# Kernel tuning notes

Hardware: AMD Instinct MI355X
Metric: run time of the kernel (lower is better)

## Reference

```python
import jax, jax.numpy as jnp
import numpy as np

NEG_BIG = -9.0e15


def masked_mean_softmax(idx):
    # softmax over a 0/-inf mask == uniform weights over positions where idx > 0
    logits = jnp.where(idx > 0, 1.0, NEG_BIG).astype(jnp.float32)
    return jax.nn.softmax(logits, axis=1)


def setup_inputs() -> dict:
    key = jax.random.key(0)
    ks = jax.random.split(key, 8)
    N_NODES, N_EDGES, EDGE_ARITY, NODE_DEG = 100000, 50000, 32, 16
    D_IN, D_OUT, TV = 128, 128, 128
    stdv = 1.0 / np.sqrt(D_IN)
    u = lambda k, shp: jax.random.uniform(k, shp, jnp.float32, -stdv, stdv)
    return {
        "x": jax.random.normal(ks[0], (N_NODES, D_IN), jnp.float32),
        "seq": jax.random.randint(ks[1], (N_EDGES, EDGE_ARITY), 0, N_NODES),
        "useq": jax.random.randint(ks[2], (N_NODES, NODE_DEG), 0, N_EDGES),
        "TextVector": jax.random.normal(ks[3], (TV,), jnp.float32),
        "weight1": u(ks[4], (D_IN, D_OUT)),
        "weight2": u(ks[5], (D_OUT, D_OUT)),
        "weight3": u(ks[6], (TV, TV)),
    }


def reference(x, seq, useq, TextVector, weight1, weight2, weight3):
    # NOTE: the torch module overwrites TextVector with weight3[0]; dropout is
    # a no-op in eval mode and is omitted here.
    tv = weight3[0]                                   # [TV]
    dot = weight3 @ tv                                # [TV]
    cos = dot / (jnp.linalg.norm(tv) * jnp.linalg.norm(weight3, axis=1))
    inter_nw = jnp.mean(cos)                          # scalar

    xw = (x @ weight1) * inter_nw                     # [N, D_OUT]

    nor = masked_mean_softmax(seq)                    # [E, A]
    adj_with_fea = xw[seq]                            # [E, A, D_OUT] gather
    edge = jnp.einsum('eac,ea->ec', adj_with_fea, nor)
    edge = jax.nn.relu(edge)
    e1 = edge @ weight2                               # [E, D_OUT]

    u_nor = masked_mean_softmax(useq)                 # [N, K]
    edge_adj = e1[useq]                               # [N, K, D_OUT] gather
    node = jnp.einsum('nkc,nk->nc', edge_adj, u_nor)  # [N, D_OUT]
    return node
```

## Files before the change

### kernel.cpp

```cpp
#include <hip/hip_runtime.h>
#include <hip/hip_fp16.h>

#define ND 100000
#define NE 50000
#define AR 32
#define DG 16
#define D  128

typedef _Float16 half8_t __attribute__((ext_vector_type(8)));
typedef _Float16 half4_t __attribute__((ext_vector_type(4)));
typedef float    f32x4_t __attribute__((ext_vector_type(4)));
typedef int      i32x4_t __attribute__((ext_vector_type(4)));

#define APAD 136

template<int OFF, int NI>
__device__ __forceinline__ void g_load8(half8_t (&v)[8], const int (&idxs)[NI],
                                        const _Float16* __restrict__ tab) {
    #pragma unroll
    for (int i = 0; i < 8; ++i)
        v[i] = *(const half8_t*)(tab + (size_t)idxs[OFF + i] * 32);
}

template<int OFF, int NI>
__device__ __forceinline__ void g_acc8(const half8_t (&v)[8], const int (&idxs)[NI],
                                       bool allv, float wv, float (&acc)[8]) {
    #pragma unroll
    for (int i = 0; i < 8; ++i) {
        float w = (allv | (idxs[OFF + i] > 0)) ? wv : 0.f;
        #pragma unroll
        for (int jj = 0; jj < 8; ++jj)
            acc[jj] = fmaf(w, (float)v[i][jj], acc[jj]);
    }
}

__global__ __launch_bounds__(256) void k_prep(const float* __restrict__ w1,
                                              const float* __restrict__ w2,
                                              const float* __restrict__ w3,
                                              _Float16* __restrict__ w1f,
                                              _Float16* __restrict__ w2f,
                                              float* __restrict__ inter_out) {
    if (blockIdx.x == 64) {
        __shared__ float red[128];
        int j = threadIdx.x;
        if (j < 128) {
            float dot = 0.f, sq = 0.f, sq0 = 0.f;
            #pragma unroll 8
            for (int k = 0; k < D; ++k) {
                float wj = w3[j * D + k];
                float w0 = w3[k];
                dot += wj * w0;
                sq  += wj * wj;
                sq0 += w0 * w0;
            }
            red[j] = dot / (sqrtf(sq0) * sqrtf(sq));
        }
        __syncthreads();
        if (j == 0) {
            float s = 0.f;
            for (int i = 0; i < 128; ++i) s += red[i];
            inter_out[0] = s / 128.f;
        }
        return;
    }
    int o = blockIdx.x * 256 + threadIdx.x;
    int j    = o & 7;
    int lane = (o >> 3) & 63;
    int frag = o >> 9;
    int ntile = frag >> 2, ktile = frag & 3;
    int n = ntile * 16 + (lane & 15);
    int k = ktile * 32 + (lane >> 4) * 8 + j;
    w1f[o] = (_Float16)w1[k * D + n];
    w2f[o] = (_Float16)w2[k * D + n];
}

__global__ __launch_bounds__(256) void k_xw(const float* __restrict__ x,
                                            const _Float16* __restrict__ w1f_g,
                                            const float* __restrict__ inter_p,
                                            _Float16* __restrict__ xws) {
    __shared__ _Float16 wfrag[D * D];
    __shared__ _Float16 xs[64 * APAD];
    int t = threadIdx.x;
    {
        const float4* src = (const float4*)w1f_g;
        float4* dst = (float4*)wfrag;
        #pragma unroll
        for (int i = 0; i < 8; ++i) dst[i * 256 + t] = src[i * 256 + t];
    }
    int rowbase = blockIdx.x * 64;
    #pragma unroll
    for (int p = 0; p < 8; ++p) {
        int idx = p * 1024 + t * 4;
        int r = idx >> 7, c = idx & 127;
        int grow = rowbase + r;
        float4 v = make_float4(0.f, 0.f, 0.f, 0.f);
        if (grow < ND) v = ((const float4*)x)[(size_t)grow * 32 + (c >> 2)];
        half4_t h = { (_Float16)v.x, (_Float16)v.y, (_Float16)v.z, (_Float16)v.w };
        *(half4_t*)&xs[r * APAD + c] = h;
    }
    __syncthreads();

    int wave = t >> 6, lane = t & 63;
    int quad = lane >> 4, l15 = lane & 15;
    int m0 = wave * 16;
    float inter = inter_p[0];

    half8_t a[4];
    #pragma unroll
    for (int kt = 0; kt < 4; ++kt)
        a[kt] = *(const half8_t*)&xs[(m0 + l15) * APAD + kt * 32 + quad * 8];

    int grow = rowbase + m0 + l15;
    #pragma unroll
    for (int nt = 0; nt < 8; ++nt) {
        f32x4_t acc = {0.f, 0.f, 0.f, 0.f};
        #pragma unroll
        for (int kt = 0; kt < 4; ++kt) {
            half8_t b = *(const half8_t*)&wfrag[((nt * 4 + kt) * 64 + lane) * 8];
            acc = __builtin_amdgcn_mfma_f32_16x16x32_f16(b, a[kt], acc, 0, 0, 0);
        }
        half4_t hv = { (_Float16)(acc[0] * inter), (_Float16)(acc[1] * inter),
                       (_Float16)(acc[2] * inter), (_Float16)(acc[3] * inter) };
        if (grow < ND)
            *(half4_t*)(xws + ((size_t)(nt >> 1) * ND + grow) * 32
                            + (nt & 1) * 16 + quad * 4) = hv;
    }
}

__global__ __launch_bounds__(256, 4) void k_gather_e(const int* __restrict__ seq,
                                                     const _Float16* __restrict__ xws,
                                                     _Float16* __restrict__ ea) {
    int t = threadIdx.x;
    int s = blockIdx.x & 3;
    int g = blockIdx.x >> 2;
    int e = t >> 2, part = t & 3;
    int eg = g * 64 + e;
    int egs = min(eg, NE - 1);

    const i32x4_t* sp = (const i32x4_t*)(seq + (size_t)egs * AR);
    i32x4_t q0 = __builtin_nontemporal_load(sp + 0);
    i32x4_t q1 = __builtin_nontemporal_load(sp + 1);
    i32x4_t q2 = __builtin_nontemporal_load(sp + 2);
    i32x4_t q3 = __builtin_nontemporal_load(sp + 3);
    i32x4_t q4 = __builtin_nontemporal_load(sp + 4);
    i32x4_t q5 = __builtin_nontemporal_load(sp + 5);
    i32x4_t q6 = __builtin_nontemporal_load(sp + 6);
    i32x4_t q7 = __builtin_nontemporal_load(sp + 7);
    int idxs[32] = { q0[0], q0[1], q0[2], q0[3], q1[0], q1[1], q1[2], q1[3],
                     q2[0], q2[1], q2[2], q2[3], q3[0], q3[1], q3[2], q3[3],
                     q4[0], q4[1], q4[2], q4[3], q5[0], q5[1], q5[2], q5[3],
                     q6[0], q6[1], q6[2], q6[3], q7[0], q7[1], q7[2], q7[3] };
    int cnt = 0;
    #pragma unroll
    for (int j = 0; j < AR; ++j) cnt += (idxs[j] > 0);
    bool allv = (cnt == 0);
    float wv = 1.f / (float)(allv ? AR : cnt);

    const _Float16* tab = xws + (size_t)s * ND * 32 + part * 8;

    float acc[8] = {};
    half8_t va[8], vb[8];
    g_load8<0>(va, idxs, tab);
    g_load8<8>(vb, idxs, tab);
    __builtin_amdgcn_sched_barrier(0);
    g_acc8<0>(va, idxs, allv, wv, acc);
    g_load8<16>(va, idxs, tab);
    __builtin_amdgcn_sched_barrier(0);
    g_acc8<8>(vb, idxs, allv, wv, acc);
    g_load8<24>(vb, idxs, tab);
    __builtin_amdgcn_sched_barrier(0);
    g_acc8<16>(va, idxs, allv, wv, acc);
    g_acc8<24>(vb, idxs, allv, wv, acc);

    if (eg < NE) {
        half8_t h;
        #pragma unroll
        for (int jj = 0; jj < 8; ++jj) h[jj] = (_Float16)fmaxf(acc[jj], 0.f);
        __builtin_nontemporal_store(h, (half8_t*)(ea + (size_t)eg * D + s * 32 + part * 8));
    }
}

__global__ __launch_bounds__(256) void k_gemm_e(const _Float16* __restrict__ ea,
                                                const _Float16* __restrict__ w2f_g,
                                                _Float16* __restrict__ e1s) {
    __shared__ _Float16 wfrag[D * D];
    __shared__ _Float16 et[64 * APAD];
    int t = threadIdx.x;
    {
        const float4* src = (const float4*)w2f_g;
        float4* dst = (float4*)wfrag;
        #pragma unroll
        for (int i = 0; i < 8; ++i) dst[i * 256 + t] = src[i * 256 + t];
    }
    int rowbase = blockIdx.x * 64;
    #pragma unroll
    for (int p = 0; p < 4; ++p) {
        int hidx = p * 2048 + t * 8;
        int r = hidx >> 7, c = hidx & 127;
        int grow = rowbase + r;
        int gs = (grow < NE) ? grow : (NE - 1);
        half8_t v = *(const half8_t*)(ea + (size_t)gs * D + c);
        *(half8_t*)&et[r * APAD + c] = v;
    }
    __syncthreads();

    int wave = t >> 6, lane = t & 63;
    int quad = lane >> 4, l15 = lane & 15;
    int m0 = wave * 16;

    half8_t a[4];
    #pragma unroll
    for (int kt = 0; kt < 4; ++kt)
        a[kt] = *(const half8_t*)&et[(m0 + l15) * APAD + kt * 32 + quad * 8];

    int grow = rowbase + m0 + l15;
    #pragma unroll
    for (int nt = 0; nt < 8; ++nt) {
        f32x4_t acc = {0.f, 0.f, 0.f, 0.f};
        #pragma unroll
        for (int kt = 0; kt < 4; ++kt) {
            half8_t b = *(const half8_t*)&wfrag[((nt * 4 + kt) * 64 + lane) * 8];
            acc = __builtin_amdgcn_mfma_f32_16x16x32_f16(b, a[kt], acc, 0, 0, 0);
        }
        half4_t hv = { (_Float16)acc[0], (_Float16)acc[1],
                       (_Float16)acc[2], (_Float16)acc[3] };
        if (grow < NE)
            *(half4_t*)(e1s + ((size_t)(nt >> 1) * NE + grow) * 32
                            + (nt & 1) * 16 + quad * 4) = hv;
    }
}

__global__ __launch_bounds__(256, 4) void k_gather_n(const int* __restrict__ useq,
                                                     const _Float16* __restrict__ e1s,
                                                     float* __restrict__ out) {
    int t = threadIdx.x;
    int s = blockIdx.x & 3;
    int g = blockIdx.x >> 2;
    int n = t >> 2, part = t & 3;
    int ng = g * 64 + n;
    int ns = min(ng, ND - 1);

    const i32x4_t* up = (const i32x4_t*)(useq + (size_t)ns * DG);
    i32x4_t q0 = __builtin_nontemporal_load(up + 0);
    i32x4_t q1 = __builtin_nontemporal_load(up + 1);
    i32x4_t q2 = __builtin_nontemporal_load(up + 2);
    i32x4_t q3 = __builtin_nontemporal_load(up + 3);
    int idxs[16] = { q0[0], q0[1], q0[2], q0[3], q1[0], q1[1], q1[2], q1[3],
                     q2[0], q2[1], q2[2], q2[3], q3[0], q3[1], q3[2], q3[3] };
    int cnt = 0;
    #pragma unroll
    for (int j = 0; j < DG; ++j) cnt += (idxs[j] > 0);
    bool allv = (cnt == 0);
    float wv = 1.f / (float)(allv ? DG : cnt);

    const _Float16* tab = e1s + (size_t)s * NE * 32 + part * 8;

    float acc[8] = {};
    half8_t va[8], vb[8];
    g_load8<0>(va, idxs, tab);
    g_load8<8>(vb, idxs, tab);
    __builtin_amdgcn_sched_barrier(0);
    g_acc8<0>(va, idxs, allv, wv, acc);
    g_acc8<8>(vb, idxs, allv, wv, acc);

    if (ng < ND) {
        f32x4_t o0 = { acc[0], acc[1], acc[2], acc[3] };
        f32x4_t o1 = { acc[4], acc[5], acc[6], acc[7] };
        f32x4_t* p = (f32x4_t*)(out + (size_t)ng * D + s * 32 + part * 8);
        __builtin_nontemporal_store(o0, p);
        __builtin_nontemporal_store(o1, p + 1);
    }
}

extern "C" void kernel_launch(void* const* d_in, const int* in_sizes, int n_in,
                              void* d_out, int out_size, void* d_ws, size_t ws_size,
                              hipStream_t stream) {
    const float* x    = (const float*)d_in[0];
    const int*   seq  = (const int*)d_in[1];
    const int*   useq = (const int*)d_in[2];
    const float* w1   = (const float*)d_in[4];
    const float* w2   = (const float*)d_in[5];
    const float* w3   = (const float*)d_in[6];
    float* out = (float*)d_out;

    _Float16* xws   = (_Float16*)d_out;
    _Float16* ea    = (_Float16*)d_out + (size_t)ND * D;
    float*    inter = (float*)d_ws;
    _Float16* w1f   = (_Float16*)((char*)d_ws + 256);
    _Float16* w2f   = (_Float16*)((char*)d_ws + 256 + 32768);
    _Float16* e1s   = (_Float16*)((char*)d_ws + 256 + 65536);

    int eg_grp = (NE + 63) / 64;
    int ng_grp = (ND + 63) / 64;

    hipLaunchKernelGGL(k_prep,     dim3(65),             dim3(256), 0, stream, w1, w2, w3, w1f, w2f, inter);
    hipLaunchKernelGGL(k_xw,       dim3((ND + 63) / 64), dim3(256), 0, stream, x, w1f, inter, xws);
    hipLaunchKernelGGL(k_gather_e, dim3(eg_grp * 4),     dim3(256), 0, stream, seq, xws, ea);
    hipLaunchKernelGGL(k_gemm_e,   dim3((NE + 63) / 64), dim3(256), 0, stream, ea, w2f, e1s);
    hipLaunchKernelGGL(k_gather_n, dim3(ng_grp * 4),     dim3(256), 0, stream, useq, e1s, out);
}
```

Measured before the change: 236.6 us.

## Reorder gather before W1 GEMM and fuse both GEMMs per edge tile

Uses linearity to apply weight1 after the edge aggregation rather than before it. The first GEMM therefore runs over 50k edges instead of 100k nodes, and the node-side xw GEMM becomes a simple scaled fp16 cast of x. Both edge GEMMs (W1 with ReLU, then W2) are fused in one kernel that reuses the LDS tile, which removes one intermediate global round trip. W2 fragments are now read straight from global memory rather than LDS, and partial sums are rounded to fp16 before the W1 product.

```diff
diff --git a/kernel.cpp b/kernel.cpp
--- a/kernel.cpp
+++ b/kernel.cpp
@@ -74,57 +74,19 @@
     w2f[o] = (_Float16)w2[k * D + n];
 }
 
-__global__ __launch_bounds__(256) void k_xw(const float* __restrict__ x,
-                                            const _Float16* __restrict__ w1f_g,
-                                            const float* __restrict__ inter_p,
-                                            _Float16* __restrict__ xws) {
-    __shared__ _Float16 wfrag[D * D];
-    __shared__ _Float16 xs[64 * APAD];
-    int t = threadIdx.x;
-    {
-        const float4* src = (const float4*)w1f_g;
-        float4* dst = (float4*)wfrag;
-        #pragma unroll
-        for (int i = 0; i < 8; ++i) dst[i * 256 + t] = src[i * 256 + t];
-    }
-    int rowbase = blockIdx.x * 64;
-    #pragma unroll
-    for (int p = 0; p < 8; ++p) {
-        int idx = p * 1024 + t * 4;
-        int r = idx >> 7, c = idx & 127;
-        int grow = rowbase + r;
-        float4 v = make_float4(0.f, 0.f, 0.f, 0.f);
-        if (grow < ND) v = ((const float4*)x)[(size_t)grow * 32 + (c >> 2)];
-        half4_t h = { (_Float16)v.x, (_Float16)v.y, (_Float16)v.z, (_Float16)v.w };
-        *(half4_t*)&xs[r * APAD + c] = h;
-    }
-    __syncthreads();
-
-    int wave = t >> 6, lane = t & 63;
-    int quad = lane >> 4, l15 = lane & 15;
-    int m0 = wave * 16;
+__global__ __launch_bounds__(256) void k_cast(const float* __restrict__ x,
+                                              const float* __restrict__ inter_p,
+                                              _Float16* __restrict__ xh) {
+    int gid = blockIdx.x * 256 + threadIdx.x;
+    int r = gid >> 5, c4 = gid & 31;
+    if (r >= ND) return;
     float inter = inter_p[0];
-
-    half8_t a[4];
-    #pragma unroll
-    for (int kt = 0; kt < 4; ++kt)
-        a[kt] = *(const half8_t*)&xs[(m0 + l15) * APAD + kt * 32 + quad * 8];
-
-    int grow = rowbase + m0 + l15;
-    #pragma unroll
-    for (int nt = 0; nt < 8; ++nt) {
-        f32x4_t acc = {0.f, 0.f, 0.f, 0.f};
-        #pragma unroll
-        for (int kt = 0; kt < 4; ++kt) {
-            half8_t b = *(const half8_t*)&wfrag[((nt * 4 + kt) * 64 + lane) * 8];
-            acc = __builtin_amdgcn_mfma_f32_16x16x32_f16(b, a[kt], acc, 0, 0, 0);
-        }
-        half4_t hv = { (_Float16)(acc[0] * inter), (_Float16)(acc[1] * inter),
-                       (_Float16)(acc[2] * inter), (_Float16)(acc[3] * inter) };
-        if (grow < ND)
-            *(half4_t*)(xws + ((size_t)(nt >> 1) * ND + grow) * 32
-                            + (nt & 1) * 16 + quad * 4) = hv;
-    }
+    float4 v = ((const float4*)x)[(size_t)r * 32 + c4];
+    int slice = c4 >> 3;
+    int cc = (c4 & 7) * 4;
+    half4_t h = { (_Float16)(v.x * inter), (_Float16)(v.y * inter),
+                  (_Float16)(v.z * inter), (_Float16)(v.w * inter) };
+    *(half4_t*)(xh + ((size_t)slice * ND + r) * 32 + cc) = h;
 }
 
 __global__ __launch_bounds__(256, 4) void k_gather_e(const int* __restrict__ seq,
@@ -175,19 +137,20 @@
     if (eg < NE) {
         half8_t h;
         #pragma unroll
-        for (int jj = 0; jj < 8; ++jj) h[jj] = (_Float16)fmaxf(acc[jj], 0.f);
-        __builtin_nontemporal_store(h, (half8_t*)(ea + (size_t)eg * D + s * 32 + part * 8));
-    }
-}
-
-__global__ __launch_bounds__(256) void k_gemm_e(const _Float16* __restrict__ ea,
-                                                const _Float16* __restrict__ w2f_g,
-                                                _Float16* __restrict__ e1s) {
+        for (int jj = 0; jj < 8; ++jj) h[jj] = (_Float16)acc[jj];
+        *(half8_t*)(ea + (size_t)eg * D + s * 32 + part * 8) = h;
+    }
+}
+
+__global__ __launch_bounds__(256) void k_gemm2(const _Float16* __restrict__ ep,
+                                               const _Float16* __restrict__ w1f_g,
+                                               const _Float16* __restrict__ w2f_g,
+                                               _Float16* __restrict__ e1s) {
     __shared__ _Float16 wfrag[D * D];
     __shared__ _Float16 et[64 * APAD];
     int t = threadIdx.x;
     {
-        const float4* src = (const float4*)w2f_g;
+        const float4* src = (const float4*)w1f_g;
         float4* dst = (float4*)wfrag;
         #pragma unroll
         for (int i = 0; i < 8; ++i) dst[i * 256 + t] = src[i * 256 + t];
@@ -199,7 +162,7 @@
         int r = hidx >> 7, c = hidx & 127;
         int grow = rowbase + r;
         int gs = (grow < NE) ? grow : (NE - 1);
-        half8_t v = *(const half8_t*)(ea + (size_t)gs * D + c);
+        half8_t v = *(const half8_t*)(ep + (size_t)gs * D + c);
         *(half8_t*)&et[r * APAD + c] = v;
     }
     __syncthreads();
@@ -213,7 +176,6 @@
     for (int kt = 0; kt < 4; ++kt)
         a[kt] = *(const half8_t*)&et[(m0 + l15) * APAD + kt * 32 + quad * 8];
 
-    int grow = rowbase + m0 + l15;
     #pragma unroll
     for (int nt = 0; nt < 8; ++nt) {
         f32x4_t acc = {0.f, 0.f, 0.f, 0.f};
@@ -221,6 +183,25 @@
         for (int kt = 0; kt < 4; ++kt) {
             half8_t b = *(const half8_t*)&wfrag[((nt * 4 + kt) * 64 + lane) * 8];
             acc = __builtin_amdgcn_mfma_f32_16x16x32_f16(b, a[kt], acc, 0, 0, 0);
+        }
+        half4_t hv = { (_Float16)fmaxf(acc[0], 0.f), (_Float16)fmaxf(acc[1], 0.f),
+                       (_Float16)fmaxf(acc[2], 0.f), (_Float16)fmaxf(acc[3], 0.f) };
+        *(half4_t*)&et[(m0 + l15) * APAD + nt * 16 + quad * 4] = hv;
+    }
+
+    half8_t a2[4];
+    #pragma unroll
+    for (int kt = 0; kt < 4; ++kt)
+        a2[kt] = *(const half8_t*)&et[(m0 + l15) * APAD + kt * 32 + quad * 8];
+
+    int grow = rowbase + m0 + l15;
+    #pragma unroll
+    for (int nt = 0; nt < 8; ++nt) {
+        f32x4_t acc = {0.f, 0.f, 0.f, 0.f};
+        #pragma unroll
+        for (int kt = 0; kt < 4; ++kt) {
+            half8_t b = *(const half8_t*)&w2f_g[((nt * 4 + kt) * 64 + lane) * 8];
+            acc = __builtin_amdgcn_mfma_f32_16x16x32_f16(b, a2[kt], acc, 0, 0, 0);
         }
         half4_t hv = { (_Float16)acc[0], (_Float16)acc[1],
                        (_Float16)acc[2], (_Float16)acc[3] };
@@ -283,8 +264,8 @@
     const float* w3   = (const float*)d_in[6];
     float* out = (float*)d_out;
 
-    _Float16* xws   = (_Float16*)d_out;
-    _Float16* ea    = (_Float16*)d_out + (size_t)ND * D;
+    _Float16* xh    = (_Float16*)d_out;
+    _Float16* ep    = (_Float16*)d_out + (size_t)ND * D;
     float*    inter = (float*)d_ws;
     _Float16* w1f   = (_Float16*)((char*)d_ws + 256);
     _Float16* w2f   = (_Float16*)((char*)d_ws + 256 + 32768);
@@ -293,9 +274,9 @@
     int eg_grp = (NE + 63) / 64;
     int ng_grp = (ND + 63) / 64;
 
-    hipLaunchKernelGGL(k_prep,     dim3(65),             dim3(256), 0, stream, w1, w2, w3, w1f, w2f, inter);
-    hipLaunchKernelGGL(k_xw,       dim3((ND + 63) / 64), dim3(256), 0, stream, x, w1f, inter, xws);
-    hipLaunchKernelGGL(k_gather_e, dim3(eg_grp * 4),     dim3(256), 0, stream, seq, xws, ea);
-    hipLaunchKernelGGL(k_gemm_e,   dim3((NE + 63) / 64), dim3(256), 0, stream, ea, w2f, e1s);
-    hipLaunchKernelGGL(k_gather_n, dim3(ng_grp * 4),     dim3(256), 0, stream, useq, e1s, out);
-}
+    hipLaunchKernelGGL(k_prep,     dim3(65),               dim3(256), 0, stream, w1, w2, w3, w1f, w2f, inter);
+    hipLaunchKernelGGL(k_cast,     dim3(ND * 32 / 256),    dim3(256), 0, stream, x, inter, xh);
+    hipLaunchKernelGGL(k_gather_e, dim3(eg_grp * 4),       dim3(256), 0, stream, seq, xh, ep);
+    hipLaunchKernelGGL(k_gemm2,    dim3(eg_grp),           dim3(256), 0, stream, ep, w1f, w2f, e1s);
+    hipLaunchKernelGGL(k_gather_n, dim3(ng_grp * 4),       dim3(256), 0, stream, useq, e1s, out);
+}
```

Measured after the change: 283.1 us. 1.2x slower.
